# Kernel tuning notes

Hardware: AMD Instinct MI355X
Metric: run time of the kernel (lower is better)

## Reference

```python
import jax, jax.numpy as jnp
import numpy as np
from jax import lax

B = 64          # batch
L = 8192        # seq_len
NB = 20         # n_pha_bands + n_amp_bands
K = 769         # padded FIR kernel length (odd), ~cycle*fs/low_hz for lowest band


def setup_inputs() -> dict:
    key = jax.random.key(0)
    kx, kk = jax.random.split(key)
    x = jax.random.normal(kx, (B, 1, L), dtype=jnp.float32)
    # stand-in for the designed+padded tensorpac FIR bank (registered buffer)
    kernels = jax.random.normal(kk, (NB, K), dtype=jnp.float32) * (1.0 / K)
    return {"x": x, "kernels": kernels}


def reference(x, kernels):
    # filtfilt_mode=True, edge_mode=None branch of BandPassFilter.forward
    nb, k = kernels.shape
    seq_len = x.shape[-1]
    padlen = min(3 * k, seq_len - 1)  # same for all bands: kernels share padded length
    xs = x[:, 0, :]  # [B, L]
    # scipy-style odd extension, vectorized over batch (replaces per-sample loop)
    left = -jnp.flip(xs[:, 1:padlen + 1], axis=-1)
    right = -jnp.flip(xs[:, -padlen - 1:-1], axis=-1)
    xp = jnp.concatenate([left, xs, right], axis=-1)[:, None, :]  # [B,1,Lp]
    same = [(k // 2, k // 2)]  # 'same' padding for odd k
    w = kernels[:, None, :]    # [NB,1,K] (OIH)
    dn = ("NCH", "OIH", "NCH")
    # forward pass: all bands at once (replaces per-band loop)
    y = lax.conv_general_dilated(xp, w, (1,), same, dimension_numbers=dn)  # [B,NB,Lp]
    # backward pass of filtfilt: flip, depthwise conv per band, flip back
    y2 = lax.conv_general_dilated(jnp.flip(y, -1), w, (1,), same,
                                  dimension_numbers=dn, feature_group_count=nb)
    y2 = jnp.flip(y2, -1)[:, :, padlen:-padlen]  # crop odd extension -> [B,NB,L]
    return y2[:, None, :, :]  # [B,1,NB,L]
```

## Files before the change

### kernel.cpp

```cpp
#include <hip/hip_runtime.h>

#define B_      64
#define L_      8192
#define NB_     20
#define K_      769
#define GLEN    1537
#define GSM     1552
#define NSTEP2  49
#define NSTEPP2 56
#define TB      512
#define CPF     1416
#define NWF     1376
#define NWB     1344
#define PADLEN  2307
#define OFFSET  1539
#define PBUF    (NB_ * GSM)

typedef _Float16 half8  __attribute__((ext_vector_type(8)));
typedef float    f32x16 __attribute__((ext_vector_type(16)));

#define MFMA(a, b, c) __builtin_amdgcn_mfma_f32_32x32x16_f16((a), (b), (c), 0, 0, 0)

__global__ __launch_bounds__(256) void bp_combine(
    const float* __restrict__ kern, float* __restrict__ gpart)
{
    __shared__ __align__(16) float ks[K_];
    const int o   = blockIdx.x;
    const int jc  = blockIdx.z;
    const int tid = threadIdx.x;
    for (int i = tid; i < K_; i += 256) ks[i] = kern[o * K_ + i];
    __syncthreads();

    const int m = blockIdx.y * 194 + tid;
    if (tid < 194 && m < GSM) {
        float acc = 0.f;
        int jlo = (m > K_ - 1) ? (m - (K_ - 1)) : 0;
        int jhi = (m < K_ - 1) ? m : (K_ - 1);
        if (jlo < jc * 193) jlo = jc * 193;
        if (jhi > jc * 193 + 192) jhi = jc * 193 + 192;
        for (int j = jlo; j <= jhi; ++j)
            acc = fmaf(ks[K_ - 1 - j], ks[m - j], acc);
        gpart[jc * PBUF + o * GSM + m] = acc;
    }
}

__global__ __launch_bounds__(256) void bp_pack(
    const float* __restrict__ gpart, _Float16* __restrict__ gbuf)
{
    const int t = blockIdx.x * 256 + threadIdx.x;
    if (t >= NSTEPP2 * 64) return;
    const int step = t >> 6;
    const int l    = t & 63;
    const int o    = l & 31;
    const int h5   = l >> 5;
    half8 f;
    #pragma unroll
    for (int e = 0; e < 8; ++e) {
        const int tap = 16 * step + 8 * h5 + e;
        float v = 0.f;
        if (o < NB_ && tap <= 768) {
            const int idx = o * GSM + tap;
            const float gg = gpart[idx] + gpart[PBUF + idx] +
                             gpart[2 * PBUF + idx] + gpart[3 * PBUF + idx];
            v = gg * (tap == 768 ? 512.0f : 1024.0f);
        }
        f[e] = (_Float16)v;
    }
    *((half8*)gbuf + t) = f;
}

__global__ __launch_bounds__(256, 2) void bp_mfma(
    const float* __restrict__ x, const _Float16* __restrict__ gbuf,
    float* __restrict__ out)
{
    __shared__ __align__(16) _Float16 xls[16 * CPF + 16];

    const int blk  = blockIdx.x;
    const int tile = blk & 15;
    const int b    = blk >> 4;
    const int tid  = threadIdx.x;
    const int l    = tid & 63;
    const int w    = tid >> 6;

    const int T0 = tile * TB;
    const int P0 = T0 + OFFSET;
    const float* __restrict__ xrow = x + b * L_;

    float fv[6], bv[6];
    #pragma unroll
    for (int r = 0; r < 6; ++r) {
        const int i = tid + 256 * r;
        if (i < NWF) {
            const int p = P0 + i;
            fv[r] = (p < PADLEN) ? -xrow[PADLEN - p]
                  : (p < PADLEN + L_) ? xrow[p - PADLEN]
                  : -xrow[(L_ - 2) + (PADLEN + L_) - p];
        }
        const int j = tid + 256 * r;
        if (j < NWB) {
            const int p = P0 + 2048 - j;
            bv[r] = (p < PADLEN) ? -xrow[PADLEN - p]
                  : (p < PADLEN + L_) ? xrow[p - PADLEN]
                  : -xrow[(L_ - 2) + (PADLEN + L_) - p];
        }
    }
    #pragma unroll
    for (int r = 0; r < 6; ++r) {
        const int i = tid + 256 * r;
        if (i < NWF) {
            const _Float16 h = (_Float16)fv[r];
            #pragma unroll
            for (int cc = 0; cc < 8; ++cc)
                if (i - cc >= 0) xls[cc * CPF + (i - cc)] = h;
        }
        const int j = tid + 256 * r;
        if (j < NWB) {
            const _Float16 h = (_Float16)bv[r];
            #pragma unroll
            for (int cc = 0; cc < 8; ++cc)
                if (j - cc >= 0) xls[(8 + cc) * CPF + (j - cc)] = h;
        }
    }
    __syncthreads();

    const int u  = l & 31;
    const int h5 = l >> 5;
    const int c  = l & 7;
    const int c2 = (-l) & 7;

    f32x16 acc[4];
    #pragma unroll
    for (int q = 0; q < 4; ++q)
        #pragma unroll
        for (int r = 0; r < 16; ++r) acc[q][r] = 0.f;

    const char* lb0  = (const char*)xls + c * (CPF * 2)
                     + 2 * (128 * w + u + 8 * h5 - c);
    const char* lbb0 = (const char*)xls + (8 + c2) * (CPF * 2)
                     + 2 * (512 - 128 * w - u + 8 * h5 - c2);

    half8 E[4], O[4], Eb[4], Ob[4];
    #pragma unroll
    for (int j = 0; j < 4; ++j) {
        E[j] = *(const half8*)(lb0 + 64 * j);
        O[j] = *(const half8*)(lb0 + 32 + 64 * j);
    }
    Eb[0] = *(const half8*)(lbb0);
    Eb[3] = *(const half8*)(lbb0 - 64);
    Eb[2] = *(const half8*)(lbb0 - 128);
    Eb[1] = *(const half8*)(lbb0 - 192);
    Ob[0] = *(const half8*)(lbb0 + 32);
    Ob[3] = *(const half8*)(lbb0 + 32 - 64);
    Ob[2] = *(const half8*)(lbb0 + 32 - 128);
    Ob[1] = *(const half8*)(lbb0 + 32 - 192);

    const half8* __restrict__ gp = (const half8*)gbuf + l;
    half8 gq[8];
    #pragma unroll
    for (int j = 0; j < 8; ++j) gq[j] = gp[64 * j];

    for (int n = 0; n < 3; ++n) {
        const char*  lbf = lb0 + 512 * n;
        const char*  lbb = lbb0 + 512 * n;
        const half8* gpn = gp + 64 * 16 * n;
        #pragma unroll
        for (int k = 0; k < 16; ++k) {
            const int gs = k & 7;
            const int ph = (k >> 1) & 3;
            __builtin_amdgcn_s_setprio(1);
            if ((k & 1) == 0) {
                acc[0] = MFMA(gq[gs], E[(ph + 0) & 3] + Eb[(ph + 4 - 0) & 3], acc[0]);
                acc[1] = MFMA(gq[gs], E[(ph + 1) & 3] + Eb[(ph + 4 - 1) & 3], acc[1]);
                acc[2] = MFMA(gq[gs], E[(ph + 2) & 3] + Eb[(ph + 4 - 2) & 3], acc[2]);
                acc[3] = MFMA(gq[gs], E[(ph + 3) & 3] + Eb[(ph + 4 - 3) & 3], acc[3]);
                __builtin_amdgcn_s_setprio(0);
                E[ph]            = *(const half8*)(lbf + 32 * k + 256);
                Eb[(ph + 1) & 3] = *(const half8*)(lbb + 32 * k + 64);
            } else {
                acc[0] = MFMA(gq[gs], O[(ph + 0) & 3] + Ob[(ph + 4 - 0) & 3], acc[0]);
                acc[1] = MFMA(gq[gs], O[(ph + 1) & 3] + Ob[(ph + 4 - 1) & 3], acc[1]);
                acc[2] = MFMA(gq[gs], O[(ph + 2) & 3] + Ob[(ph + 4 - 2) & 3], acc[2]);
                acc[3] = MFMA(gq[gs], O[(ph + 3) & 3] + Ob[(ph + 4 - 3) & 3], acc[3]);
                __builtin_amdgcn_s_setprio(0);
                O[ph]            = *(const half8*)(lbf + 32 * k + 256);
                Ob[(ph + 1) & 3] = *(const half8*)(lbb + 32 * k + 64);
            }
            gq[gs] = gpn[64 * (k + 8)];
        }
    }

    __builtin_amdgcn_s_setprio(1);
    acc[0] = MFMA(gq[0], E[0] + Eb[0], acc[0]);
    acc[1] = MFMA(gq[0], E[1] + Eb[3], acc[1]);
    acc[2] = MFMA(gq[0], E[2] + Eb[2], acc[2]);
    acc[3] = MFMA(gq[0], E[3] + Eb[1], acc[3]);
    __builtin_amdgcn_s_setprio(0);

    const float sc = 1.0f / 1024.0f;
    #pragma unroll
    for (int q = 0; q < 4; ++q) {
        const int tb = T0 + 128 * w + 32 * q + u;
        #pragma unroll
        for (int r = 0; r < 16; ++r) {
            const int o = (r & 3) + 8 * (r >> 2) + 4 * h5;
            if (o < NB_)
                __builtin_nontemporal_store(acc[q][r] * sc,
                                            &out[((b * NB_ + o) << 13) + tb]);
        }
    }
}

extern "C" void kernel_launch(void* const* d_in, const int* in_sizes, int n_in,
                              void* d_out, int out_size, void* d_ws, size_t ws_size,
                              hipStream_t stream)
{
    const float* x    = (const float*)d_in[0];
    const float* kern = (const float*)d_in[1];
    float*       out  = (float*)d_out;

    float*    gpart = (float*)d_ws;
    _Float16* gbuf  = (_Float16*)((char*)d_ws + 496640);

    bp_combine<<<dim3(NB_, 8, 4), 256, 0, stream>>>(kern, gpart);
    bp_pack<<<14, 256, 0, stream>>>(gpart, gbuf);
    bp_mfma<<<B_ * (L_ / TB), 256, 0, stream>>>(x, gbuf, out);
}
```

Baseline: 46.94 us.

## Stage FIR weights in LDS via async global_load_lds and halve shifted x copies

Filter-bank fragments (gbuf) are now copied into shared memory with asynchronous global_load_lds at kernel start, and the MFMA loop reads them from LDS with a two-deep register double buffer instead of an eight-deep global prefetch. The shifted copies of the input window drop from 8 to 4 per direction, and fragment reads become two 8-byte LDS loads to handle the resulting 8-byte alignment. The intent is to remove global-memory latency from the inner loop and cut LDS fill work, at the cost of more LDS per block (~46KB, which may affect occupancy) and twice as many LDS load instructions.

Result: faster. 45.47 us (-3.1%).

```diff
diff --git a/kernel.cpp b/kernel.cpp
--- a/kernel.cpp
+++ b/kernel.cpp
@@ -9,17 +9,26 @@
 #define NSTEP2  49
 #define NSTEPP2 56
 #define TB      512
-#define CPF     1416
-#define NWF     1376
-#define NWB     1344
+#define CPF4    1360
+#define NWS     1320
+#define XBOFF   (4 * CPF4)
+#define GOFF    (8 * CPF4)
+#define LDS_H   (8 * CPF4 + NSTEP2 * 512)
 #define PADLEN  2307
 #define OFFSET  1539
 #define PBUF    (NB_ * GSM)
 
+typedef _Float16 half4  __attribute__((ext_vector_type(4)));
 typedef _Float16 half8  __attribute__((ext_vector_type(8)));
 typedef float    f32x16 __attribute__((ext_vector_type(16)));
 
 #define MFMA(a, b, c) __builtin_amdgcn_mfma_f32_32x32x16_f16((a), (b), (c), 0, 0, 0)
+
+__device__ __forceinline__ half8 ld_h8(const char* p) {
+    const half4 lo = *(const half4*)p;
+    const half4 hi = *(const half4*)(p + 8);
+    return __builtin_shufflevector(lo, hi, 0, 1, 2, 3, 4, 5, 6, 7);
+}
 
 __global__ __launch_bounds__(256) void bp_combine(
     const float* __restrict__ kern, float* __restrict__ gpart)
@@ -73,7 +82,7 @@
     const float* __restrict__ x, const _Float16* __restrict__ gbuf,
     float* __restrict__ out)
 {
-    __shared__ __align__(16) _Float16 xls[16 * CPF + 16];
+    __shared__ __align__(16) _Float16 lds[LDS_H];
 
     const int blk  = blockIdx.x;
     const int tile = blk & 15;
@@ -85,48 +94,55 @@
     const int T0 = tile * TB;
     const int P0 = T0 + OFFSET;
     const float* __restrict__ xrow = x + b * L_;
+    const char*  __restrict__ gsrc = (const char*)gbuf;
+
+    #pragma unroll
+    for (int it = 0; it < 13; ++it) {
+        const int idx = it * 256 + tid;
+        if (idx < NSTEP2 * 64) {
+            __builtin_amdgcn_global_load_lds(
+                (const __attribute__((address_space(1))) void*)(gsrc + (size_t)idx * 16),
+                (__attribute__((address_space(3))) void*)&lds[GOFF + (size_t)(it * 256 + (tid & 192)) * 8],
+                16, 0, 0);
+        }
+    }
 
     float fv[6], bv[6];
     #pragma unroll
     for (int r = 0; r < 6; ++r) {
         const int i = tid + 256 * r;
-        if (i < NWF) {
+        if (i < NWS) {
             const int p = P0 + i;
             fv[r] = (p < PADLEN) ? -xrow[PADLEN - p]
                   : (p < PADLEN + L_) ? xrow[p - PADLEN]
                   : -xrow[(L_ - 2) + (PADLEN + L_) - p];
-        }
-        const int j = tid + 256 * r;
-        if (j < NWB) {
-            const int p = P0 + 2048 - j;
-            bv[r] = (p < PADLEN) ? -xrow[PADLEN - p]
-                  : (p < PADLEN + L_) ? xrow[p - PADLEN]
-                  : -xrow[(L_ - 2) + (PADLEN + L_) - p];
+            const int p2 = P0 + 2048 - i;
+            bv[r] = (p2 < PADLEN) ? -xrow[PADLEN - p2]
+                  : (p2 < PADLEN + L_) ? xrow[p2 - PADLEN]
+                  : -xrow[(L_ - 2) + (PADLEN + L_) - p2];
         }
     }
     #pragma unroll
     for (int r = 0; r < 6; ++r) {
         const int i = tid + 256 * r;
-        if (i < NWF) {
-            const _Float16 h = (_Float16)fv[r];
+        if (i < NWS) {
+            const _Float16 hf = (_Float16)fv[r];
+            const _Float16 hb = (_Float16)bv[r];
             #pragma unroll
-            for (int cc = 0; cc < 8; ++cc)
-                if (i - cc >= 0) xls[cc * CPF + (i - cc)] = h;
-        }
-        const int j = tid + 256 * r;
-        if (j < NWB) {
-            const _Float16 h = (_Float16)bv[r];
-            #pragma unroll
-            for (int cc = 0; cc < 8; ++cc)
-                if (j - cc >= 0) xls[(8 + cc) * CPF + (j - cc)] = h;
+            for (int cc = 0; cc < 4; ++cc) {
+                if (i - cc >= 0) {
+                    lds[cc * CPF4 + (i - cc)] = hf;
+                    lds[XBOFF + cc * CPF4 + (i - cc)] = hb;
+                }
+            }
         }
     }
     __syncthreads();
 
     const int u  = l & 31;
     const int h5 = l >> 5;
-    const int c  = l & 7;
-    const int c2 = (-l) & 7;
+    const int c4f = u & 3;
+    const int c4b = (512 - u) & 3;
 
     f32x16 acc[4];
     #pragma unroll
@@ -134,58 +150,55 @@
         #pragma unroll
         for (int r = 0; r < 16; ++r) acc[q][r] = 0.f;
 
-    const char* lb0  = (const char*)xls + c * (CPF * 2)
-                     + 2 * (128 * w + u + 8 * h5 - c);
-    const char* lbb0 = (const char*)xls + (8 + c2) * (CPF * 2)
-                     + 2 * (512 - 128 * w - u + 8 * h5 - c2);
+    const char* ldsb = (const char*)lds;
+    const char* lbf0 = ldsb + 2 * (c4f * CPF4 + (128 * w + u + 8 * h5 - c4f));
+    const char* lbb0 = ldsb + 2 * (XBOFF + c4b * CPF4 + (512 - 128 * w - u + 8 * h5 - c4b));
+    const char* gpl  = ldsb + 2 * GOFF + l * 16;
 
     half8 E[4], O[4], Eb[4], Ob[4];
     #pragma unroll
     for (int j = 0; j < 4; ++j) {
-        E[j] = *(const half8*)(lb0 + 64 * j);
-        O[j] = *(const half8*)(lb0 + 32 + 64 * j);
-    }
-    Eb[0] = *(const half8*)(lbb0);
-    Eb[3] = *(const half8*)(lbb0 - 64);
-    Eb[2] = *(const half8*)(lbb0 - 128);
-    Eb[1] = *(const half8*)(lbb0 - 192);
-    Ob[0] = *(const half8*)(lbb0 + 32);
-    Ob[3] = *(const half8*)(lbb0 + 32 - 64);
-    Ob[2] = *(const half8*)(lbb0 + 32 - 128);
-    Ob[1] = *(const half8*)(lbb0 + 32 - 192);
-
-    const half8* __restrict__ gp = (const half8*)gbuf + l;
-    half8 gq[8];
-    #pragma unroll
-    for (int j = 0; j < 8; ++j) gq[j] = gp[64 * j];
+        E[j] = ld_h8(lbf0 + 64 * j);
+        O[j] = ld_h8(lbf0 + 32 + 64 * j);
+    }
+    Eb[0] = ld_h8(lbb0);
+    Eb[3] = ld_h8(lbb0 - 64);
+    Eb[2] = ld_h8(lbb0 - 128);
+    Eb[1] = ld_h8(lbb0 - 192);
+    Ob[0] = ld_h8(lbb0 + 32);
+    Ob[3] = ld_h8(lbb0 + 32 - 64);
+    Ob[2] = ld_h8(lbb0 + 32 - 128);
+    Ob[1] = ld_h8(lbb0 + 32 - 192);
+
+    half8 gq[2];
+    gq[0] = *(const half8*)(gpl);
 
     for (int n = 0; n < 3; ++n) {
-        const char*  lbf = lb0 + 512 * n;
-        const char*  lbb = lbb0 + 512 * n;
-        const half8* gpn = gp + 64 * 16 * n;
+        const char* lbf = lbf0 + 512 * n;
+        const char* lbb = lbb0 + 512 * n;
+        const char* gst = gpl + 16384 * n;
         #pragma unroll
         for (int k = 0; k < 16; ++k) {
-            const int gs = k & 7;
             const int ph = (k >> 1) & 3;
+            gq[(k + 1) & 1] = *(const half8*)(gst + (k + 1) * 1024);
             __builtin_amdgcn_s_setprio(1);
             if ((k & 1) == 0) {
-                acc[0] = MFMA(gq[gs], E[(ph + 0) & 3] + Eb[(ph + 4 - 0) & 3], acc[0]);
-                acc[1] = MFMA(gq[gs], E[(ph + 1) & 3] + Eb[(ph + 4 - 1) & 3], acc[1]);
-                acc[2] = MFMA(gq[gs], E[(ph + 2) & 3] + Eb[(ph + 4 - 2) & 3], acc[2]);
-                acc[3] = MFMA(gq[gs], E[(ph + 3) & 3] + Eb[(ph + 4 - 3) & 3], acc[3]);
+                acc[0] = MFMA(gq[k & 1], E[(ph + 0) & 3] + Eb[(ph + 4 - 0) & 3], acc[0]);
+                acc[1] = MFMA(gq[k & 1], E[(ph + 1) & 3] + Eb[(ph + 4 - 1) & 3], acc[1]);
+                acc[2] = MFMA(gq[k & 1], E[(ph + 2) & 3] + Eb[(ph + 4 - 2) & 3], acc[2]);
+                acc[3] = MFMA(gq[k & 1], E[(ph + 3) & 3] + Eb[(ph + 4 - 3) & 3], acc[3]);
                 __builtin_amdgcn_s_setprio(0);
-                E[ph]            = *(const half8*)(lbf + 32 * k + 256);
-                Eb[(ph + 1) & 3] = *(const half8*)(lbb + 32 * k + 64);
+                E[ph]            = ld_h8(lbf + 32 * k + 256);
+                Eb[(ph + 1) & 3] = ld_h8(lbb + 32 * k + 64);
             } else {
-                acc[0] = MFMA(gq[gs], O[(ph + 0) & 3] + Ob[(ph + 4 - 0) & 3], acc[0]);
-                acc[1] = MFMA(gq[gs], O[(ph + 1) & 3] + Ob[(ph + 4 - 1) & 3], acc[1]);
-                acc[2] = MFMA(gq[gs], O[(ph + 2) & 3] + Ob[(ph + 4 - 2) & 3], acc[2]);
-                acc[3] = MFMA(gq[gs], O[(ph + 3) & 3] + Ob[(ph + 4 - 3) & 3], acc[3]);
+                acc[0] = MFMA(gq[k & 1], O[(ph + 0) & 3] + Ob[(ph + 4 - 0) & 3], acc[0]);
+                acc[1] = MFMA(gq[k & 1], O[(ph + 1) & 3] + Ob[(ph + 4 - 1) & 3], acc[1]);
+                acc[2] = MFMA(gq[k & 1], O[(ph + 2) & 3] + Ob[(ph + 4 - 2) & 3], acc[2]);
+                acc[3] = MFMA(gq[k & 1], O[(ph + 3) & 3] + Ob[(ph + 4 - 3) & 3], acc[3]);
                 __builtin_amdgcn_s_setprio(0);
-                O[ph]            = *(const half8*)(lbf + 32 * k + 256);
-                Ob[(ph + 1) & 3] = *(const half8*)(lbb + 32 * k + 64);
+                O[ph]            = ld_h8(lbf + 32 * k + 256);
+                Ob[(ph + 1) & 3] = ld_h8(lbb + 32 * k + 64);
             }
-            gq[gs] = gpn[64 * (k + 8)];
         }
     }
 
```

## Switch Toeplitz MFMA from 32x32x16 to 16x16x32 tiles with two band groups

Applied to the files above, without the earlier changes.

Replaces the 32x32x16 MFMA formulation with 16x16x32 MFMAs. The 20 bands are split into two 16-row groups, and each wave covers its 128 output positions as eight 16-column tiles. The coefficient packing, LDS staging layout, backward-window offsets and register rotation all change to match the K=32 step. The aim is to cut the waste of padding 20 bands up to 32 rows. In exchange it issues more MFMA instructions (the second band group is only a quarter used) and needs more register arrays.

After: 45.33 us. -3.4%, faster.

```diff
diff --git a/kernel.cpp b/kernel.cpp
--- a/kernel.cpp
+++ b/kernel.cpp
@@ -6,20 +6,23 @@
 #define K_      769
 #define GLEN    1537
 #define GSM     1552
-#define NSTEP2  49
-#define NSTEPP2 56
+#define NST3    25
+#define NSTP3   28
 #define TB      512
-#define CPF     1416
-#define NWF     1376
-#define NWB     1344
+#define CPF     1360
+#define CPB     1472
+#define NWF     1360
+#define NWB     1472
+#define XB      (8 * CPF)
+#define LDS_H   (8 * CPF + 8 * CPB)
 #define PADLEN  2307
 #define OFFSET  1539
 #define PBUF    (NB_ * GSM)
 
 typedef _Float16 half8  __attribute__((ext_vector_type(8)));
-typedef float    f32x16 __attribute__((ext_vector_type(16)));
-
-#define MFMA(a, b, c) __builtin_amdgcn_mfma_f32_32x32x16_f16((a), (b), (c), 0, 0, 0)
+typedef float    f32x4  __attribute__((ext_vector_type(4)));
+
+#define MFMA16(a, b, c) __builtin_amdgcn_mfma_f32_16x16x32_f16((a), (b), (c), 0, 0, 0)
 
 __global__ __launch_bounds__(256) void bp_combine(
     const float* __restrict__ kern, float* __restrict__ gpart)
@@ -48,15 +51,16 @@
     const float* __restrict__ gpart, _Float16* __restrict__ gbuf)
 {
     const int t = blockIdx.x * 256 + threadIdx.x;
-    if (t >= NSTEPP2 * 64) return;
-    const int step = t >> 6;
+    if (t >= NSTP3 * 2 * 64) return;
     const int l    = t & 63;
-    const int o    = l & 31;
-    const int h5   = l >> 5;
+    const int tau  = (t >> 6) & 1;
+    const int step = t >> 7;
+    const int g4   = l >> 4;
+    const int o    = 16 * tau + (l & 15);
     half8 f;
     #pragma unroll
     for (int e = 0; e < 8; ++e) {
-        const int tap = 16 * step + 8 * h5 + e;
+        const int tap = 32 * step + 8 * g4 + e;
         float v = 0.f;
         if (o < NB_ && tap <= 768) {
             const int idx = o * GSM + tap;
@@ -73,7 +77,7 @@
     const float* __restrict__ x, const _Float16* __restrict__ gbuf,
     float* __restrict__ out)
 {
-    __shared__ __align__(16) _Float16 xls[16 * CPF + 16];
+    __shared__ __align__(16) _Float16 lds[LDS_H];
 
     const int blk  = blockIdx.x;
     const int tile = blk & 15;
@@ -96,12 +100,11 @@
                   : (p < PADLEN + L_) ? xrow[p - PADLEN]
                   : -xrow[(L_ - 2) + (PADLEN + L_) - p];
         }
-        const int j = tid + 256 * r;
-        if (j < NWB) {
-            const int p = P0 + 2048 - j;
-            bv[r] = (p < PADLEN) ? -xrow[PADLEN - p]
-                  : (p < PADLEN + L_) ? xrow[p - PADLEN]
-                  : -xrow[(L_ - 2) + (PADLEN + L_) - p];
+        if (i < NWB) {
+            const int p2 = P0 + 2160 - i;
+            bv[r] = (p2 < PADLEN) ? -xrow[PADLEN - p2]
+                  : (p2 < PADLEN + L_) ? xrow[p2 - PADLEN]
+                  : -xrow[(L_ - 2) + (PADLEN + L_) - p2];
         }
     }
     #pragma unroll
@@ -111,101 +114,99 @@
             const _Float16 h = (_Float16)fv[r];
             #pragma unroll
             for (int cc = 0; cc < 8; ++cc)
-                if (i - cc >= 0) xls[cc * CPF + (i - cc)] = h;
-        }
-        const int j = tid + 256 * r;
-        if (j < NWB) {
+                if (i - cc >= 0) lds[cc * CPF + (i - cc)] = h;
+        }
+        if (i < NWB) {
             const _Float16 h = (_Float16)bv[r];
             #pragma unroll
             for (int cc = 0; cc < 8; ++cc)
-                if (j - cc >= 0) xls[(8 + cc) * CPF + (j - cc)] = h;
+                if (i - cc >= 0) lds[XB + cc * CPB + (i - cc)] = h;
         }
     }
     __syncthreads();
 
-    const int u  = l & 31;
-    const int h5 = l >> 5;
-    const int c  = l & 7;
-    const int c2 = (-l) & 7;
-
-    f32x16 acc[4];
-    #pragma unroll
-    for (int q = 0; q < 4; ++q)
+    const int g4 = l >> 4;
+    const int t4 = l & 15;
+    const int cf = l & 7;
+    const int cb = (16 - t4) & 7;
+
+    f32x4 acc0[8], acc1[8];
+    #pragma unroll
+    for (int q = 0; q < 8; ++q) {
+        acc0[q] = (f32x4){0.f, 0.f, 0.f, 0.f};
+        acc1[q] = (f32x4){0.f, 0.f, 0.f, 0.f};
+    }
+
+    const int base_f = 128 * w + t4 + 8 * g4;
+    const int base_b = 624 - 128 * w - t4 + 8 * g4;
+    const char* lbf0 = (const char*)lds + 2 * (cf * CPF + (base_f - cf));
+    const char* lbb0 = (const char*)lds + 2 * (XB + cb * CPB + (base_b - cb));
+
+    half8 R[8], Rb[8];
+    #pragma unroll
+    for (int a = 0; a < 8; ++a)
+        R[a] = *(const half8*)(lbf0 + 32 * a);
+    Rb[0] = *(const half8*)(lbb0);
+    #pragma unroll
+    for (int j = 1; j < 8; ++j)
+        Rb[j] = *(const half8*)(lbb0 - 32 * (8 - j));
+
+    const half8* __restrict__ gp = (const half8*)gbuf + l;
+    half8 ga[2][2];
+    ga[0][0] = gp[0];   ga[0][1] = gp[64];
+    ga[1][0] = gp[128]; ga[1][1] = gp[192];
+
+    for (int n = 0; n < 6; ++n) {
+        const char* lbf = lbf0 + 256 * n;
+        const char* lbb = lbb0 + 256 * n;
+        const half8* gpn = gp + 128 * 4 * n;
         #pragma unroll
-        for (int r = 0; r < 16; ++r) acc[q][r] = 0.f;
-
-    const char* lb0  = (const char*)xls + c * (CPF * 2)
-                     + 2 * (128 * w + u + 8 * h5 - c);
-    const char* lbb0 = (const char*)xls + (8 + c2) * (CPF * 2)
-                     + 2 * (512 - 128 * w - u + 8 * h5 - c2);
-
-    half8 E[4], O[4], Eb[4], Ob[4];
-    #pragma unroll
-    for (int j = 0; j < 4; ++j) {
-        E[j] = *(const half8*)(lb0 + 64 * j);
-        O[j] = *(const half8*)(lb0 + 32 + 64 * j);
-    }
-    Eb[0] = *(const half8*)(lbb0);
-    Eb[3] = *(const half8*)(lbb0 - 64);
-    Eb[2] = *(const half8*)(lbb0 - 128);
-    Eb[1] = *(const half8*)(lbb0 - 192);
-    Ob[0] = *(const half8*)(lbb0 + 32);
-    Ob[3] = *(const half8*)(lbb0 + 32 - 64);
-    Ob[2] = *(const half8*)(lbb0 + 32 - 128);
-    Ob[1] = *(const half8*)(lbb0 + 32 - 192);
-
-    const half8* __restrict__ gp = (const half8*)gbuf + l;
-    half8 gq[8];
-    #pragma unroll
-    for (int j = 0; j < 8; ++j) gq[j] = gp[64 * j];
-
-    for (int n = 0; n < 3; ++n) {
-        const char*  lbf = lb0 + 512 * n;
-        const char*  lbb = lbb0 + 512 * n;
-        const half8* gpn = gp + 64 * 16 * n;
+        for (int k4 = 0; k4 < 4; ++k4) {
+            const int p = 2 * k4;
+            const int sel = k4 & 1;
+            __builtin_amdgcn_s_setprio(1);
+            #pragma unroll
+            for (int q = 0; q < 8; ++q) {
+                const half8 Bq = R[(p + q) & 7] + Rb[(p + 8 - q) & 7];
+                acc0[q] = MFMA16(ga[sel][0], Bq, acc0[q]);
+                acc1[q] = MFMA16(ga[sel][1], Bq, acc1[q]);
+            }
+            __builtin_amdgcn_s_setprio(0);
+            R[p & 7]        = *(const half8*)(lbf + 64 * k4 + 256);
+            R[(p + 1) & 7]  = *(const half8*)(lbf + 64 * k4 + 288);
+            Rb[(p + 1) & 7] = *(const half8*)(lbb + 64 * k4 + 32);
+            Rb[(p + 2) & 7] = *(const half8*)(lbb + 64 * k4 + 64);
+            ga[sel][0] = gpn[(k4 + 2) * 128];
+            ga[sel][1] = gpn[(k4 + 2) * 128 + 64];
+        }
+    }
+
+    __builtin_amdgcn_s_setprio(1);
+    #pragma unroll
+    for (int q = 0; q < 8; ++q) {
+        const half8 Bq = R[q & 7] + Rb[(8 - q) & 7];
+        acc0[q] = MFMA16(ga[0][0], Bq, acc0[q]);
+        acc1[q] = MFMA16(ga[0][1], Bq, acc1[q]);
+    }
+    __builtin_amdgcn_s_setprio(0);
+
+    const float sc = 1.0f / 1024.0f;
+    #pragma unroll
+    for (int q = 0; q < 8; ++q) {
+        const int tb = T0 + 128 * w + 16 * q + t4;
         #pragma unroll
-        for (int k = 0; k < 16; ++k) {
-            const int gs = k & 7;
-            const int ph = (k >> 1) & 3;
-            __builtin_amdgcn_s_setprio(1);
-            if ((k & 1) == 0) {
-                acc[0] = MFMA(gq[gs], E[(ph + 0) & 3] + Eb[(ph + 4 - 0) & 3], acc[0]);
-                acc[1] = MFMA(gq[gs], E[(ph + 1) & 3] + Eb[(ph + 4 - 1) & 3], acc[1]);
-                acc[2] = MFMA(gq[gs], E[(ph + 2) & 3] + Eb[(ph + 4 - 2) & 3], acc[2]);
-                acc[3] = MFMA(gq[gs], E[(ph + 3) & 3] + Eb[(ph + 4 - 3) & 3], acc[3]);
-                __builtin_amdgcn_s_setprio(0);
-                E[ph]            = *(const half8*)(lbf + 32 * k + 256);
-                Eb[(ph + 1) & 3] = *(const half8*)(lbb + 32 * k + 64);
-            } else {
-                acc[0] = MFMA(gq[gs], O[(ph + 0) & 3] + Ob[(ph + 4 - 0) & 3], acc[0]);
-                acc[1] = MFMA(gq[gs], O[(ph + 1) & 3] + Ob[(ph + 4 - 1) & 3], acc[1]);
-                acc[2] = MFMA(gq[gs], O[(ph + 2) & 3] + Ob[(ph + 4 - 2) & 3], acc[2]);
-                acc[3] = MFMA(gq[gs], O[(ph + 3) & 3] + Ob[(ph + 4 - 3) & 3], acc[3]);
-                __builtin_amdgcn_s_setprio(0);
-                O[ph]            = *(const half8*)(lbf + 32 * k + 256);
-                Ob[(ph + 1) & 3] = *(const half8*)(lbb + 32 * k + 64);
+        for (int r = 0; r < 4; ++r) {
+            const int o0 = 4 * g4 + r;
+            __builtin_nontemporal_store(acc0[q][r] * sc,
+                                        &out[((b * NB_ + o0) << 13) + tb]);
+        }
+        if (g4 == 0) {
+            #pragma unroll
+            for (int r = 0; r < 4; ++r) {
+                const int o1 = 16 + r;
+                __builtin_nontemporal_store(acc1[q][r] * sc,
+                                            &out[((b * NB_ + o1) << 13) + tb]);
             }
-            gq[gs] = gpn[64 * (k + 8)];
-        }
-    }
-
-    __builtin_amdgcn_s_setprio(1);
-    acc[0] = MFMA(gq[0], E[0] + Eb[0], acc[0]);
-    acc[1] = MFMA(gq[0], E[1] + Eb[3], acc[1]);
-    acc[2] = MFMA(gq[0], E[2] + Eb[2], acc[2]);
-    acc[3] = MFMA(gq[0], E[3] + Eb[1], acc[3]);
-    __builtin_amdgcn_s_setprio(0);
-
-    const float sc = 1.0f / 1024.0f;
-    #pragma unroll
-    for (int q = 0; q < 4; ++q) {
-        const int tb = T0 + 128 * w + 32 * q + u;
-        #pragma unroll
-        for (int r = 0; r < 16; ++r) {
-            const int o = (r & 3) + 8 * (r >> 2) + 4 * h5;
-            if (o < NB_)
-                __builtin_nontemporal_store(acc[q][r] * sc,
-                                            &out[((b * NB_ + o) << 13) + tb]);
         }
     }
 }
```

## Halve output tile per block and raise occupancy in MFMA kernel

Applied to the files above, without the earlier changes.

Shrinks the output tile per block from 512 to 256 samples, which doubles the grid and cuts LDS per block. Launch bounds are raised to four blocks per SM. Each wave now holds two accumulators instead of four, and the g-coefficient prefetch depth drops from 8 to 2, reducing register pressure. The trade-off is more redundant halo loading per output, since the 768-tap overlap is amortized over fewer outputs, and less register reuse of the filter fragments across accumulators.

After: 48.23 us. +2.7%, slower.

```diff
diff --git a/kernel.cpp b/kernel.cpp
--- a/kernel.cpp
+++ b/kernel.cpp
@@ -8,10 +8,12 @@
 #define GSM     1552
 #define NSTEP2  49
 #define NSTEPP2 56
-#define TB      512
-#define CPF     1416
-#define NWF     1376
-#define NWB     1344
+#define TB      256
+#define CPF     1136
+#define NWF     1120
+#define NWB     1056
+#define XB      (8 * CPF)
+#define LDS_H   (16 * CPF)
 #define PADLEN  2307
 #define OFFSET  1539
 #define PBUF    (NB_ * GSM)
@@ -69,15 +71,15 @@
     *((half8*)gbuf + t) = f;
 }
 
-__global__ __launch_bounds__(256, 2) void bp_mfma(
+__global__ __launch_bounds__(256, 4) void bp_mfma(
     const float* __restrict__ x, const _Float16* __restrict__ gbuf,
     float* __restrict__ out)
 {
-    __shared__ __align__(16) _Float16 xls[16 * CPF + 16];
+    __shared__ __align__(16) _Float16 lds[LDS_H];
 
     const int blk  = blockIdx.x;
-    const int tile = blk & 15;
-    const int b    = blk >> 4;
+    const int tile = blk & 31;
+    const int b    = blk >> 5;
     const int tid  = threadIdx.x;
     const int l    = tid & 63;
     const int w    = tid >> 6;
@@ -86,9 +88,9 @@
     const int P0 = T0 + OFFSET;
     const float* __restrict__ xrow = x + b * L_;
 
-    float fv[6], bv[6];
-    #pragma unroll
-    for (int r = 0; r < 6; ++r) {
+    float fv[5], bv[5];
+    #pragma unroll
+    for (int r = 0; r < 5; ++r) {
         const int i = tid + 256 * r;
         if (i < NWF) {
             const int p = P0 + i;
@@ -96,54 +98,52 @@
                   : (p < PADLEN + L_) ? xrow[p - PADLEN]
                   : -xrow[(L_ - 2) + (PADLEN + L_) - p];
         }
-        const int j = tid + 256 * r;
-        if (j < NWB) {
-            const int p = P0 + 2048 - j;
-            bv[r] = (p < PADLEN) ? -xrow[PADLEN - p]
-                  : (p < PADLEN + L_) ? xrow[p - PADLEN]
-                  : -xrow[(L_ - 2) + (PADLEN + L_) - p];
-        }
-    }
-    #pragma unroll
-    for (int r = 0; r < 6; ++r) {
+        if (i < NWB) {
+            const int p2 = P0 + 1792 - i;
+            bv[r] = (p2 < PADLEN) ? -xrow[PADLEN - p2]
+                  : (p2 < PADLEN + L_) ? xrow[p2 - PADLEN]
+                  : -xrow[(L_ - 2) + (PADLEN + L_) - p2];
+        }
+    }
+    #pragma unroll
+    for (int r = 0; r < 5; ++r) {
         const int i = tid + 256 * r;
         if (i < NWF) {
             const _Float16 h = (_Float16)fv[r];
             #pragma unroll
             for (int cc = 0; cc < 8; ++cc)
-                if (i - cc >= 0) xls[cc * CPF + (i - cc)] = h;
-        }
-        const int j = tid + 256 * r;
-        if (j < NWB) {
+                if (i - cc >= 0) lds[cc * CPF + (i - cc)] = h;
+        }
+        if (i < NWB) {
             const _Float16 h = (_Float16)bv[r];
             #pragma unroll
             for (int cc = 0; cc < 8; ++cc)
-                if (j - cc >= 0) xls[(8 + cc) * CPF + (j - cc)] = h;
+                if (i - cc >= 0) lds[XB + cc * CPF + (i - cc)] = h;
         }
     }
     __syncthreads();
 
     const int u  = l & 31;
     const int h5 = l >> 5;
-    const int c  = l & 7;
-    const int c2 = (-l) & 7;
-
-    f32x16 acc[4];
-    #pragma unroll
-    for (int q = 0; q < 4; ++q)
+    const int cf = u & 7;
+    const int cb = (8 - cf) & 7;
+
+    f32x16 acc[2];
+    #pragma unroll
+    for (int q = 0; q < 2; ++q)
         #pragma unroll
         for (int r = 0; r < 16; ++r) acc[q][r] = 0.f;
 
-    const char* lb0  = (const char*)xls + c * (CPF * 2)
-                     + 2 * (128 * w + u + 8 * h5 - c);
-    const char* lbb0 = (const char*)xls + (8 + c2) * (CPF * 2)
-                     + 2 * (512 - 128 * w - u + 8 * h5 - c2);
+    const int base_f = 64 * w + u + 8 * h5;
+    const int base_b = 256 - 64 * w - u + 8 * h5;
+    const char* lbf0 = (const char*)lds + 2 * (cf * CPF + (base_f - cf));
+    const char* lbb0 = (const char*)lds + 2 * (XB + cb * CPF + (base_b - cb));
 
     half8 E[4], O[4], Eb[4], Ob[4];
     #pragma unroll
     for (int j = 0; j < 4; ++j) {
-        E[j] = *(const half8*)(lb0 + 64 * j);
-        O[j] = *(const half8*)(lb0 + 32 + 64 * j);
+        E[j] = *(const half8*)(lbf0 + 64 * j);
+        O[j] = *(const half8*)(lbf0 + 32 + 64 * j);
     }
     Eb[0] = *(const half8*)(lbb0);
     Eb[3] = *(const half8*)(lbb0 - 64);
@@ -155,51 +155,45 @@
     Ob[1] = *(const half8*)(lbb0 + 32 - 192);
 
     const half8* __restrict__ gp = (const half8*)gbuf + l;
-    half8 gq[8];
-    #pragma unroll
-    for (int j = 0; j < 8; ++j) gq[j] = gp[64 * j];
+    half8 gq[2];
+    gq[0] = gp[0];
+    gq[1] = gp[64];
 
     for (int n = 0; n < 3; ++n) {
-        const char*  lbf = lb0 + 512 * n;
+        const char*  lbf = lbf0 + 512 * n;
         const char*  lbb = lbb0 + 512 * n;
         const half8* gpn = gp + 64 * 16 * n;
         #pragma unroll
         for (int k = 0; k < 16; ++k) {
-            const int gs = k & 7;
             const int ph = (k >> 1) & 3;
+            const int gs = k & 1;
             __builtin_amdgcn_s_setprio(1);
             if ((k & 1) == 0) {
-                acc[0] = MFMA(gq[gs], E[(ph + 0) & 3] + Eb[(ph + 4 - 0) & 3], acc[0]);
-                acc[1] = MFMA(gq[gs], E[(ph + 1) & 3] + Eb[(ph + 4 - 1) & 3], acc[1]);
-                acc[2] = MFMA(gq[gs], E[(ph + 2) & 3] + Eb[(ph + 4 - 2) & 3], acc[2]);
-                acc[3] = MFMA(gq[gs], E[(ph + 3) & 3] + Eb[(ph + 4 - 3) & 3], acc[3]);
+                acc[0] = MFMA(gq[gs], E[ph] + Eb[ph], acc[0]);
+                acc[1] = MFMA(gq[gs], E[(ph + 1) & 3] + Eb[(ph + 3) & 3], acc[1]);
                 __builtin_amdgcn_s_setprio(0);
                 E[ph]            = *(const half8*)(lbf + 32 * k + 256);
                 Eb[(ph + 1) & 3] = *(const half8*)(lbb + 32 * k + 64);
             } else {
-                acc[0] = MFMA(gq[gs], O[(ph + 0) & 3] + Ob[(ph + 4 - 0) & 3], acc[0]);
-                acc[1] = MFMA(gq[gs], O[(ph + 1) & 3] + Ob[(ph + 4 - 1) & 3], acc[1]);
-                acc[2] = MFMA(gq[gs], O[(ph + 2) & 3] + Ob[(ph + 4 - 2) & 3], acc[2]);
-                acc[3] = MFMA(gq[gs], O[(ph + 3) & 3] + Ob[(ph + 4 - 3) & 3], acc[3]);
+                acc[0] = MFMA(gq[gs], O[ph] + Ob[ph], acc[0]);
+                acc[1] = MFMA(gq[gs], O[(ph + 1) & 3] + Ob[(ph + 3) & 3], acc[1]);
                 __builtin_amdgcn_s_setprio(0);
                 O[ph]            = *(const half8*)(lbf + 32 * k + 256);
                 Ob[(ph + 1) & 3] = *(const half8*)(lbb + 32 * k + 64);
             }
-            gq[gs] = gpn[64 * (k + 8)];
+            gq[gs] = gpn[64 * (k + 2)];
         }
     }
 
     __builtin_amdgcn_s_setprio(1);
     acc[0] = MFMA(gq[0], E[0] + Eb[0], acc[0]);
     acc[1] = MFMA(gq[0], E[1] + Eb[3], acc[1]);
-    acc[2] = MFMA(gq[0], E[2] + Eb[2], acc[2]);
-    acc[3] = MFMA(gq[0], E[3] + Eb[1], acc[3]);
     __builtin_amdgcn_s_setprio(0);
 
     const float sc = 1.0f / 1024.0f;
     #pragma unroll
-    for (int q = 0; q < 4; ++q) {
-        const int tb = T0 + 128 * w + 32 * q + u;
+    for (int q = 0; q < 2; ++q) {
+        const int tb = T0 + 64 * w + 32 * q + u;
         #pragma unroll
         for (int r = 0; r < 16; ++r) {
             const int o = (r & 3) + 8 * (r >> 2) + 4 * h5;
```
